# Performance work log

Measured on AMD Instinct MI355X. Metric: run time of the kernel, lower is better.

The kernel has to match this reference:

```python
import jax, jax.numpy as jnp
import numpy as np

B, C, T, Q = 4, 64, 128, 128   # batch, channels (emb_dim), frames, freq bins
K = 8                          # unfold kernel size (stride 1)
H = 128                        # SRU hidden size per direction
D_IN = C * K                   # SRU input size after unfold
L = Q - K + 1                  # unfolded sequence length
EPS = 1e-5


def setup_inputs() -> dict:
    key = jax.random.key(0)
    ks = jax.random.split(key, 6)
    s = 0.02
    return {
        "features": jax.random.normal(ks[0], (B, C, T, Q), jnp.float32),
        "ln_gamma": jnp.ones((C,), jnp.float32),
        "ln_beta": jnp.zeros((C,), jnp.float32),
        # SRU per-direction weights: W maps D_IN -> [x_tilde | f_gate | r_gate | highway], each H wide
        "w_fwd": jax.random.normal(ks[1], (D_IN, 4 * H), jnp.float32) * s,
        "b_fwd": jnp.zeros((2 * H,), jnp.float32),   # [b_f | b_r]
        "w_bwd": jax.random.normal(ks[2], (D_IN, 4 * H), jnp.float32) * s,
        "b_bwd": jnp.zeros((2 * H,), jnp.float32),
        # ConvTranspose1d weight in PyTorch layout [in_ch=2H, out_ch=C, K]
        "ct_w": jax.random.normal(ks[3], (2 * H, C, K), jnp.float32) * s,
        "ct_b": jnp.zeros((C,), jnp.float32),
    }


def _sru_dir(seq, W, b, reverse):
    """One SRU direction. seq: [N, L, D_IN] -> h: [N, L, H].
    c_t = f_t*c_{t-1} + (1-f_t)*x~_t ;  h_t = r_t*tanh(c_t) + (1-r_t)*x'_t
    (x' is the highway projection since input dim != hidden dim)."""
    U = seq @ W                                   # [N, L, 4H] -- dominant GEMM
    xt, f_pre, r_pre, xp = jnp.split(U, 4, axis=-1)
    bf, br = jnp.split(b, 2)
    f = jax.nn.sigmoid(f_pre + bf)
    r = jax.nn.sigmoid(r_pre + br)
    u = (1.0 - f) * xt
    if reverse:
        f = jnp.flip(f, 1)
        u = jnp.flip(u, 1)
    def combine(x, y):  # linear recurrence c = a*c_prev + b, y is the later element
        return (x[0] * y[0], x[1] * y[0] + y[1])
    c = jax.lax.associative_scan(combine, (f, u), axis=1)[1]
    if reverse:
        c = jnp.flip(c, 1)
    return r * jnp.tanh(c) + (1.0 - r) * xp


def reference(features, ln_gamma, ln_beta, w_fwd, b_fwd, w_bwd, b_bwd, ct_w, ct_b):
    # LayerNorm([C,1,1]): normalize over channel dim per (b,t,q)
    mu = jnp.mean(features, axis=1, keepdims=True)
    var = jnp.var(features, axis=1, keepdims=True)
    x = (features - mu) * jax.lax.rsqrt(var + EPS)
    x = x * ln_gamma[None, :, None, None] + ln_beta[None, :, None, None]

    N = B * T
    x = x.transpose(0, 2, 1, 3).reshape(N, C, Q)          # [B*T, C, Q]
    # nn.Unfold((K,1), stride 1): channel-major patch layout -> [N, C*K, L]
    u = jnp.stack([x[:, :, i:i + L] for i in range(K)], axis=2).reshape(N, C * K, L)
    seq = u.transpose(0, 2, 1)                            # [N, L, C*K]

    h = jnp.concatenate(
        [_sru_dir(seq, w_fwd, b_fwd, False), _sru_dir(seq, w_bwd, b_bwd, True)],
        axis=-1,
    )                                                      # [N, L, 2H]

    # ConvTranspose1d(2H -> C, K, stride=1) == full correlation with flipped kernel
    rhs = jnp.flip(ct_w, -1).transpose(1, 0, 2)           # [C, 2H, K]
    y = jax.lax.conv_general_dilated(
        h.transpose(0, 2, 1), rhs, (1,), [(K - 1, K - 1)],
        dimension_numbers=("NCH", "OIH", "NCH"),
    ) + ct_b[None, :, None]                               # [N, C, Q]

    y = y.reshape(B, T, C, Q).transpose(0, 2, 1, 3)       # [B, C, T, Q]
    return y + features
```

## Files before the change

### kernel.cpp

```cpp
#include <hip/hip_runtime.h>
#include <math.h>

#define BB 4
#define CC 64
#define TT 128
#define QQ 128
#define KK 8
#define HH 128
#define NN 512
#define LL 121
#define LPAD 135

typedef unsigned short ushort;
typedef __attribute__((ext_vector_type(8))) short short8;
typedef __attribute__((ext_vector_type(4))) float f32x4;
typedef __attribute__((ext_vector_type(4))) float float4v;

#define GLP(p) ((const __attribute__((address_space(1))) void*)(p))
#define LDP(p) ((__attribute__((address_space(3))) void*)(p))

__device__ __forceinline__ ushort f2bf(float x) {
  unsigned u = __float_as_uint(x);
  unsigned r = (u + 0x7FFFu + ((u >> 16) & 1u)) >> 16;
  return (ushort)r;
}

__global__ __launch_bounds__(256)
void prep_all(const float* __restrict__ f, const float* __restrict__ gamma,
              const float* __restrict__ beta, const float* __restrict__ wf,
              const float* __restrict__ wb, const float* __restrict__ ctw,
              ushort* __restrict__ xT, ushort* __restrict__ Wt,
              ushort* __restrict__ Bct, ushort* __restrict__ zpage) {
  int bid = blockIdx.x, tid = threadIdx.x;
  if (bid < 256) {
    int p = bid * 256 + tid;
    int q = p & (QQ - 1);
    int t = (p >> 7) & (TT - 1);
    int b = p >> 14;
    const float* base = f + (size_t)b * CC * TT * QQ + (size_t)t * QQ + q;
    float v[64];
#pragma unroll
    for (int c = 0; c < 64; ++c) v[c] = base[(size_t)c * TT * QQ];
    float s = 0.f, s2 = 0.f;
#pragma unroll
    for (int c = 0; c < 64; ++c) { s += v[c]; s2 += v[c] * v[c]; }
    float mu = s * (1.f / CC);
    float var = s2 * (1.f / CC) - mu * mu;
    float rs = rsqrtf(var + 1e-5f);
    int n = b * TT + t;
    ushort* dst = xT + (size_t)n * (CC * QQ) + (size_t)q * CC;
#pragma unroll
    for (int v8 = 0; v8 < 8; ++v8) {
      short8 ov;
#pragma unroll
      for (int e = 0; e < 8; ++e) {
        int c = v8 * 8 + e;
        ov[e] = (short)f2bf((v[c] - mu) * rs * gamma[c] + beta[c]);
      }
      *(short8*)(dst + v8 * 8) = ov;
    }
  } else if (bid < 2816) {
    int idx = (bid - 256) * 256 + tid;
    if (idx < 524288) {
      int r = idx >> 9, d = idx & 511;
      int k = d >> 6, c = d & 63;
      int dir = r >> 9, t = r & 511;
      int h = (t >> 7) * 32 + ((t >> 6) & 1) * 16 + (t & 15);
      int quad = (t >> 4) & 3;
      const float* w = dir ? wb : wf;
      Wt[idx] = f2bf(w[(size_t)(c * 8 + k) * 512 + quad * 128 + h]);
    } else {
      int i2 = idx - 524288;
      int c = i2 >> 11, d = i2 & 2047;
      int k = d >> 8, j = d & 255;
      Bct[i2] = f2bf(ctw[(size_t)j * (CC * KK) + c * KK + k]);
    }
  } else {
    if (tid < 128) ((unsigned*)zpage)[tid] = 0u;
  }
}

__global__ __launch_bounds__(256, 2)
void gemm_mfma(const ushort* __restrict__ xT, const ushort* __restrict__ Wt,
               const float* __restrict__ b_fwd, const float* __restrict__ b_bwd,
               ushort* __restrict__ hp, int n0) {
  __shared__ __align__(16) char smem[49152];
  ushort* As = (ushort*)smem;
  ushort* Bs = (ushort*)(smem + 16384);

  int tid = threadIdx.x;
  int nl = blockIdx.y;
  int r0 = blockIdx.x * 256;
  int lane = tid & 63, w = tid >> 6;
  int lrow = lane & 15, lk = lane >> 4;
  f32x4 acc[8][4] = {};
  const ushort* xTn = xT + (size_t)(n0 + nl) * (CC * QQ);
  for (int ks = 0; ks < 8; ++ks) {
    if (ks) __syncthreads();
#pragma unroll
    for (int i = 0; i < 4; ++i) {
      int p = i * 256 + tid;
      int row = p >> 3, s = (p & 7) ^ (row & 7);
      int grow = ((row & 0x0C) << 3) | ((row & 0x70) >> 2) | (row & 3);
      const ushort* g = xTn + (size_t)(grow + ks) * CC + s * 8;
      ushort* l = &As[(size_t)(i * 256 + (tid & 192)) * 8];
      __builtin_amdgcn_global_load_lds(GLP(g), LDP(l), 16, 0, 0);
    }
#pragma unroll
    for (int i = 0; i < 8; ++i) {
      int p = i * 256 + tid;
      int row = p >> 3, s = (p & 7) ^ (row & 7);
      const ushort* g = Wt + (size_t)(r0 + row) * 512 + ks * 64 + s * 8;
      ushort* l = &Bs[(size_t)(i * 256 + (tid & 192)) * 8];
      __builtin_amdgcn_global_load_lds(GLP(g), LDP(l), 16, 0, 0);
    }
    __syncthreads();
#pragma unroll
    for (int s = 0; s < 2; ++s) {
      short8 a[8], b[4];
#pragma unroll
      for (int m = 0; m < 8; ++m) {
        int r = m * 16 + lrow;
        int slot = (s * 4 + lk) ^ (r & 7);
        a[m] = *(const short8*)&As[r * 64 + slot * 8];
      }
#pragma unroll
      for (int nn = 0; nn < 4; ++nn) {
        int j = w * 64 + nn * 16 + lrow;
        int slot = (s * 4 + lk) ^ (j & 7);
        b[nn] = *(const short8*)&Bs[j * 64 + slot * 8];
      }
#pragma unroll
      for (int m = 0; m < 8; ++m)
#pragma unroll
        for (int nn = 0; nn < 4; ++nn)
          acc[m][nn] = __builtin_amdgcn_mfma_f32_16x16x32_bf16(
              a[m], b[nn], acc[m][nn], 0, 0, 0);
    }
  }
  int dirf = r0 >> 9;
  int hgroup = ((r0 & 511) >> 7) + (w >> 1);
  int h = hgroup * 32 + (w & 1) * 16 + lrow;
  const float* bias = dirf ? b_bwd : b_fwd;
  float bf = bias[h], br = bias[128 + h];

  float F = 1.f, U = 0.f;
  if (dirf == 0) {
#pragma unroll
    for (int m = 0; m < 8; ++m)
#pragma unroll
      for (int g = 0; g < 4; ++g) {
        int l = lk * 32 + m * 4 + g;
        float xt = acc[m][0][g], fp = acc[m][1][g];
        float fg = 1.f / (1.f + __expf(-(fp + bf)));
        float u = (1.f - fg) * xt;
        if (l > 120) { fg = 1.f; u = 0.f; }
        U = fg * U + u;
        F = fg * F;
        acc[m][0][g] = F; acc[m][1][g] = U;
      }
  } else {
#pragma unroll
    for (int m = 7; m >= 0; --m)
#pragma unroll
      for (int g = 3; g >= 0; --g) {
        int l = lk * 32 + m * 4 + g;
        float xt = acc[m][0][g], fp = acc[m][1][g];
        float fg = 1.f / (1.f + __expf(-(fp + bf)));
        float u = (1.f - fg) * xt;
        if (l > 120) { fg = 1.f; u = 0.f; }
        U = fg * U + u;
        F = fg * F;
        acc[m][0][g] = F; acc[m][1][g] = U;
      }
  }
  int e = dirf ? 3 - lk : lk;
  float lpU = 0.f;
#pragma unroll
  for (int j = 0; j < 4; ++j) {
    int jl = dirf ? 3 - j : j;
    float tF = __shfl(F, (jl << 4) + lrow);
    float tU = __shfl(U, (jl << 4) + lrow);
    if (j < e) lpU = tF * lpU + tU;
  }
  float cinit = lpU;
  ushort* hpn = hp + (size_t)nl * LPAD * 256;
  int colbase = dirf * 128 + hgroup * 32 + (w & 1) * 16;
#pragma unroll
  for (int m = 0; m < 8; ++m) {
#pragma unroll
    for (int g = 0; g < 4; ++g) {
      int l = lk * 32 + m * 4 + g;
      float c = acc[m][1][g] + acc[m][0][g] * cinit;
      float rp = acc[m][2][g];
      float rg = 1.f / (1.f + __expf(-(rp + br)));
      float e2 = __expf(2.f * c);
      float th = (e2 - 1.f) / (e2 + 1.f);
      float ho = rg * th + (1.f - rg) * acc[m][3][g];
      hpn[(size_t)(l + 7) * 256 + colbase + lrow] = f2bf(ho);
    }
  }
}

__global__ __launch_bounds__(256)
void conv_mfma(const ushort* __restrict__ hp, const ushort* __restrict__ Bct,
               const ushort* __restrict__ zpage, const float* __restrict__ ctb,
               const float* __restrict__ feat, float* __restrict__ out, int n0) {
  __shared__ __align__(16) ushort Hs[144 * 128];
  __shared__ __align__(16) ushort Bs[2][64 * 64];
  int tid = threadIdx.x;
  int nl = blockIdx.x;
  int lane = tid & 63, w = tid >> 6;
  int wr0 = (w >> 1) * 64, wc0 = (w & 1) * 32;
  int lrow = lane & 15, lk = lane >> 4;
  f32x4 acc[4][2] = {};
  const ushort* hpn = hp + (size_t)nl * LPAD * 256;

#define CONV_BSTAGE(T, BSEL)                                               \
  {                                                                        \
    int kk_ = (T) >> 1, sub_ = (T) & 1;                                    \
    _Pragma("unroll")                                                      \
    for (int i = 0; i < 2; ++i) {                                          \
      int p = i * 256 + tid;                                               \
      int row = p >> 3, ds = p & 7;                                        \
      const ushort* g = Bct + (size_t)row * 2048 + kk_ * 256 + jh * 128    \
                      + sub_ * 64 + (ds ^ (row & 7)) * 8;                  \
      ushort* l = &Bs[BSEL][(size_t)(i * 256 + (tid & 192)) * 8];          \
      __builtin_amdgcn_global_load_lds(GLP(g), LDP(l), 16, 0, 0);          \
    }                                                                      \
  }

  for (int jh = 0; jh < 2; ++jh) {
#pragma unroll
    for (int r = 0; r < 9; ++r) {
      int p = r * 256 + tid;
      int row = p >> 4, ds = p & 15;
      int cs = (ds & 8) | ((ds & 7) ^ (row & 7));
      const ushort* g = ((unsigned)(row - 7) <= 120u)
          ? hpn + (size_t)row * 256 + jh * 128 + cs * 8
          : zpage;
      ushort* l = &Hs[(size_t)(r * 256 + (tid & 192)) * 8];
      __builtin_amdgcn_global_load_lds(GLP(g), LDP(l), 16, 0, 0);
    }
    CONV_BSTAGE(0, 0);
    __syncthreads();
    for (int t = 0; t < 16; ++t) {
      int cur = t & 1;
      if (t < 15) CONV_BSTAGE(t + 1, cur ^ 1);
      int kk = t >> 1, sub = t & 1;
#pragma unroll
      for (int s = 0; s < 2; ++s) {
        short8 a[4], b[2];
#pragma unroll
        for (int m = 0; m < 4; ++m) {
          int row = wr0 + m * 16 + lrow + 7 - kk;
          int slot = (sub * 8) | ((s * 4 + lk) ^ (row & 7));
          a[m] = *(const short8*)&Hs[row * 128 + slot * 8];
        }
#pragma unroll
        for (int nn = 0; nn < 2; ++nn) {
          int c = wc0 + nn * 16 + lrow;
          int slot = (s * 4 + lk) ^ (c & 7);
          b[nn] = *(const short8*)&Bs[cur][c * 64 + slot * 8];
        }
#pragma unroll
        for (int m = 0; m < 4; ++m)
#pragma unroll
          for (int nn = 0; nn < 2; ++nn)
            acc[m][nn] = __builtin_amdgcn_mfma_f32_16x16x32_bf16(
                a[m], b[nn], acc[m][nn], 0, 0, 0);
      }
      __syncthreads();
    }
  }
#undef CONV_BSTAGE
  int n = n0 + nl;
  int b = n >> 7, t = n & 127;
#pragma unroll
  for (int m = 0; m < 4; ++m) {
    int q0 = wr0 + m * 16 + lk * 4;
#pragma unroll
    for (int nn = 0; nn < 2; ++nn) {
      int c = wc0 + nn * 16 + lrow;
      size_t idx = (size_t)b * (CC * TT * QQ) + (size_t)c * (TT * QQ)
                 + (size_t)t * QQ + q0;
      float4v fv = *(const float4v*)&feat[idx];
      float cb = ctb[c];
      float4v ov;
#pragma unroll
      for (int g = 0; g < 4; ++g) ov[g] = acc[m][nn][g] + cb + fv[g];
      *(float4v*)&out[idx] = ov;
    }
  }
}

extern "C" void kernel_launch(void* const* d_in, const int* in_sizes, int n_in,
                              void* d_out, int out_size, void* d_ws, size_t ws_size,
                              hipStream_t stream) {
  const float* feat  = (const float*)d_in[0];
  const float* gamma = (const float*)d_in[1];
  const float* beta  = (const float*)d_in[2];
  const float* w_fwd = (const float*)d_in[3];
  const float* b_fwd = (const float*)d_in[4];
  const float* w_bwd = (const float*)d_in[5];
  const float* b_bwd = (const float*)d_in[6];
  const float* ct_w  = (const float*)d_in[7];
  const float* ct_b  = (const float*)d_in[8];
  float* out = (float*)d_out;

  char* wsb = (char*)d_ws;
  ushort* xT  = (ushort*)wsb;
  ushort* Wt  = (ushort*)(wsb + 8388608);
  ushort* Bct = (ushort*)(wsb + 9437184);
  ushort* zpg = (ushort*)(wsb + 9699328);
  size_t persist = 9699840;
  size_t per_n = 69120u;
  int NC = 4;
  for (int cand = 512; cand >= 4; cand >>= 1) {
    if (persist + (size_t)cand * per_n <= ws_size) { NC = cand; break; }
  }
  ushort* hpc = (ushort*)(wsb + persist);

  prep_all<<<dim3(2817), dim3(256), 0, stream>>>(feat, gamma, beta, w_fwd,
                                                 w_bwd, ct_w, xT, Wt, Bct, zpg);

  for (int n0 = 0; n0 < NN; n0 += NC) {
    gemm_mfma<<<dim3(4, NC), dim3(256), 0, stream>>>(xT, Wt, b_fwd, b_bwd,
                                                     hpc, n0);
    conv_mfma<<<dim3(NC), dim3(256), 0, stream>>>(hpc, Bct, zpg, ct_b, feat,
                                                  out, n0);
  }
}
```

Baseline: 123.4 us.

## Load unfold activation tile into LDS once and reuse across all K shifts

```diff
diff --git a/kernel.cpp b/kernel.cpp
--- a/kernel.cpp
+++ b/kernel.cpp
@@ -84,9 +84,9 @@
 void gemm_mfma(const ushort* __restrict__ xT, const ushort* __restrict__ Wt,
                const float* __restrict__ b_fwd, const float* __restrict__ b_bwd,
                ushort* __restrict__ hp, int n0) {
-  __shared__ __align__(16) char smem[49152];
-  ushort* As = (ushort*)smem;
-  ushort* Bs = (ushort*)(smem + 16384);
+  __shared__ __align__(16) char smem[51200];
+  ushort* Hs = (ushort*)smem;
+  ushort* Bs = (ushort*)(smem + 18432);
 
   int tid = threadIdx.x;
   int nl = blockIdx.y;
@@ -95,34 +95,51 @@
   int lrow = lane & 15, lk = lane >> 4;
   f32x4 acc[8][4] = {};
   const ushort* xTn = xT + (size_t)(n0 + nl) * (CC * QQ);
+
+#pragma unroll
+  for (int i = 0; i < 4; ++i) {
+    int p = i * 256 + tid;
+    int row = p >> 3, s3 = p & 7;
+    int key = ((row >> 3) ^ row) & 7;
+    const ushort* g = xTn + (size_t)row * CC + (s3 ^ key) * 8;
+    ushort* l = &Hs[(size_t)(i * 256 + (tid & 192)) * 8];
+    __builtin_amdgcn_global_load_lds(GLP(g), LDP(l), 16, 0, 0);
+  }
+  if (tid < 128) {
+    int p = 1024 + tid;
+    int row = p >> 3, s3 = p & 7;
+    int srow = row < 135 ? row : 134;
+    int key = ((row >> 3) ^ row) & 7;
+    const ushort* g = xTn + (size_t)srow * CC + (s3 ^ key) * 8;
+    ushort* l = &Hs[(size_t)(1024 + (tid & 64)) * 8];
+    __builtin_amdgcn_global_load_lds(GLP(g), LDP(l), 16, 0, 0);
+  }
+
+#define GEMM_BSTAGE(KS)                                                   \
+  {                                                                       \
+    _Pragma("unroll")                                                     \
+    for (int i = 0; i < 8; ++i) {                                         \
+      int p = i * 256 + tid;                                              \
+      int row = p >> 3, s3 = (p & 7) ^ (row & 7);                         \
+      const ushort* g = Wt + (size_t)(r0 + row) * 512 + (KS) * 64 + s3 * 8; \
+      ushort* l = &Bs[(size_t)(i * 256 + (tid & 192)) * 8];               \
+      __builtin_amdgcn_global_load_lds(GLP(g), LDP(l), 16, 0, 0);         \
+    }                                                                     \
+  }
+
+  GEMM_BSTAGE(0);
+  __syncthreads();
+  int RLb = ((lrow & 0x0C) << 3) | (lrow & 3);
   for (int ks = 0; ks < 8; ++ks) {
-    if (ks) __syncthreads();
-#pragma unroll
-    for (int i = 0; i < 4; ++i) {
-      int p = i * 256 + tid;
-      int row = p >> 3, s = (p & 7) ^ (row & 7);
-      int grow = ((row & 0x0C) << 3) | ((row & 0x70) >> 2) | (row & 3);
-      const ushort* g = xTn + (size_t)(grow + ks) * CC + s * 8;
-      ushort* l = &As[(size_t)(i * 256 + (tid & 192)) * 8];
-      __builtin_amdgcn_global_load_lds(GLP(g), LDP(l), 16, 0, 0);
-    }
-#pragma unroll
-    for (int i = 0; i < 8; ++i) {
-      int p = i * 256 + tid;
-      int row = p >> 3, s = (p & 7) ^ (row & 7);
-      const ushort* g = Wt + (size_t)(r0 + row) * 512 + ks * 64 + s * 8;
-      ushort* l = &Bs[(size_t)(i * 256 + (tid & 192)) * 8];
-      __builtin_amdgcn_global_load_lds(GLP(g), LDP(l), 16, 0, 0);
-    }
-    __syncthreads();
 #pragma unroll
     for (int s = 0; s < 2; ++s) {
       short8 a[8], b[4];
 #pragma unroll
       for (int m = 0; m < 8; ++m) {
-        int r = m * 16 + lrow;
-        int slot = (s * 4 + lk) ^ (r & 7);
-        a[m] = *(const short8*)&As[r * 64 + slot * 8];
+        int R = RLb + m * 4 + ks;
+        int key = ((R >> 3) ^ R) & 7;
+        int slot = (s * 4 + lk) ^ key;
+        a[m] = *(const short8*)&Hs[R * 64 + slot * 8];
       }
 #pragma unroll
       for (int nn = 0; nn < 4; ++nn) {
@@ -137,7 +154,14 @@
           acc[m][nn] = __builtin_amdgcn_mfma_f32_16x16x32_bf16(
               a[m], b[nn], acc[m][nn], 0, 0, 0);
     }
-  }
+    if (ks < 7) {
+      __syncthreads();
+      GEMM_BSTAGE(ks + 1);
+      __syncthreads();
+    }
+  }
+#undef GEMM_BSTAGE
+
   int dirf = r0 >> 9;
   int hgroup = ((r0 & 511) >> 7) + (w >> 1);
   int h = hgroup * 32 + (w & 1) * 16 + lrow;
@@ -310,10 +334,10 @@
 
   char* wsb = (char*)d_ws;
   ushort* xT  = (ushort*)wsb;
-  ushort* Wt  = (ushort*)(wsb + 8388608);
-  ushort* Bct = (ushort*)(wsb + 9437184);
-  ushort* zpg = (ushort*)(wsb + 9699328);
-  size_t persist = 9699840;
+  ushort* Wt  = (ushort*)(wsb + 8389632);
+  ushort* Bct = (ushort*)(wsb + 9438208);
+  ushort* zpg = (ushort*)(wsb + 9700352);
+  size_t persist = 9700864;
   size_t per_n = 69120u;
   int NC = 4;
   for (int cand = 512; cand >= 4; cand >>= 1) {
```

Result: no change. 121.7 us (-1.4%).
